# Kernel tuning notes

Hardware: AMD Instinct MI355X
Metric: run time of the kernel (lower is better)

Reference implementation:

```python
import jax, jax.numpy as jnp
import numpy as np

B, V, N = 256, 50, 32
D, H, L, CS, NN, OUT = 128, 384, 12, 10, 10000, 128
ND = N * D          # per-visit input dim
G = 4 * H + 2 * L   # gate projection width
CH = H // L         # chunk size
HS = H // 6         # scale bottleneck


def setup_inputs() -> dict:
    key = jax.random.key(0)
    ks = jax.random.split(key, 20)
    s = 0.02
    embed = jax.random.normal(ks[0], (NN + 1, D), jnp.float32) * s
    embed = embed.at[0].set(0.0)  # padding_idx=0
    inp = {
        'node_ids': jax.random.randint(ks[1], (B, V, N), 0, NN + 1),
        'edge_idx': jax.random.randint(ks[2], (2, 128), 0, NN),
        'edge_attr': jax.random.normal(ks[3], (128,), jnp.float32),
        'time': jax.random.uniform(ks[4], (B, V), jnp.float32),
        'visit_order': jax.random.randint(ks[5], (B, V), 0, V),
        'attn_mask': jnp.ones((B, V), jnp.bool_),
        'embed': embed,
        'kernel_w': jax.random.normal(ks[6], (G, ND + 1), jnp.float32) * s,
        'kernel_b': jnp.zeros((G,), jnp.float32),
        'rec_w': jax.random.normal(ks[7], (G, H + 1), jnp.float32) * s,
        'rec_b': jnp.zeros((G,), jnp.float32),
        'scale_w': jax.random.normal(ks[8], (HS, H), jnp.float32) * s,
        'scale_b': jnp.zeros((HS,), jnp.float32),
        'rescale_w': jax.random.normal(ks[9], (H, HS), jnp.float32) * s,
        'rescale_b': jnp.zeros((H,), jnp.float32),
        'conv_w': jax.random.normal(ks[10], (H, H, CS), jnp.float32) * s,
        'conv_b': jnp.zeros((H,), jnp.float32),
        'out_w': jax.random.normal(ks[11], (OUT, V * H), jnp.float32) * s,
        'out_b': jnp.zeros((OUT,), jnp.float32),
    }
    return inp


def _cumax_l2r(x):
    return jnp.cumsum(jax.nn.softmax(x, -1), -1)


def _cumax_r2l(x):
    return jnp.flip(jnp.cumsum(jax.nn.softmax(jnp.flip(x, -1), -1), -1), -1)


def _forward(node_ids, time, embed, kernel_w, kernel_b, rec_w, rec_b,
             scale_w, scale_b, rescale_w, rescale_b, conv_w, conv_b, out_w, out_b):
    x = embed[node_ids].reshape(B, V, ND)  # gather per-visit code embeddings

    def step(carry, xs):
        c, h, tmp_h, tmp_dis = carry
        x_t, t_t = xs
        iv = t_t[:, None]
        xo = (jnp.concatenate([x_t, iv], -1) @ kernel_w.T + kernel_b
              + jnp.concatenate([h, iv], -1) @ rec_w.T + rec_b)
        fm = _cumax_l2r(xo[:, :L])              # [B,L] master forget
        im = _cumax_r2l(xo[:, L:2 * L])         # [B,L] master input
        g = xo[:, 2 * L:].reshape(B, 4 * L, CH)
        f = jax.nn.sigmoid(g[:, :L])
        i_ = jax.nn.sigmoid(g[:, L:2 * L])
        o = jax.nn.sigmoid(g[:, 2 * L:3 * L])
        cin = jnp.tanh(g[:, 3 * L:])
        cl = c.reshape(B, L, CH)
        fmE, imE = fm[:, :, None], im[:, :, None]
        ov = fmE * imE
        cnew = ov * (f * cl + i_ * cin) + (fmE - ov) * cl + (imE - ov) * cin
        hnew = (o * jnp.tanh(cnew)).reshape(B, H)
        cnew = cnew.reshape(B, H)
        dist = 1.0 - jnp.mean(fm, -1)           # [B]
        tmp_h = jnp.concatenate([tmp_h[1:], hnew[None]], 0)    # [CS,B,H]
        tmp_dis = jnp.concatenate([tmp_dis[1:], dist[None]], 0)  # [CS,B]
        ld = jax.nn.softmax(jnp.cumsum(tmp_dis.T, 1), 1)       # [B,CS]
        lh = tmp_h.transpose(1, 2, 0) * ld[:, None, :]         # [B,H,CS]
        theme = jax.nn.sigmoid(
            jnp.maximum(jnp.mean(lh, -1) @ scale_w.T + scale_b, 0.0)
            @ rescale_w.T + rescale_b)
        conv = jnp.einsum('bhk,ohk->bo', lh, conv_w) + conv_b  # valid conv, len 1
        local = theme * conv
        return (cnew, hnew, tmp_h, tmp_dis), (local, hnew, dist)

    c0 = jnp.zeros((B, H), jnp.float32)
    h0 = jnp.zeros((B, H), jnp.float32)
    tmp_h0 = jnp.zeros((CS, B, H), jnp.float32)
    tmp_dis0 = jnp.zeros((CS, B), jnp.float32)
    xs = (x.transpose(1, 0, 2), time.T)
    _, (hs, ohs, dists) = jax.lax.scan(step, (c0, h0, tmp_h0, tmp_dis0), xs)
    rnn = hs.transpose(1, 0, 2) + ohs.transpose(1, 0, 2)       # [B,V,H]
    out = rnn.reshape(B, V * H) @ out_w.T + out_b
    return out, dists  # dists: [V,B]


def reference(node_ids, edge_idx, edge_attr, time, visit_order, attn_mask,
              embed, kernel_w, kernel_b, rec_w, rec_b, scale_w, scale_b,
              rescale_w, rescale_b, conv_w, conv_b, out_w, out_b):
    # edge_idx / edge_attr / visit_order / attn_mask are unused by StageNet.forward
    return _forward(node_ids, time, embed, kernel_w, kernel_b, rec_w, rec_b,
                    scale_w, scale_b, rescale_w, rescale_b, conv_w, conv_b,
                    out_w, out_b)
```

## Files before the change

### kernel.cpp

```cpp
#include <hip/hip_runtime.h>
#include <math.h>

typedef _Float16 f16;
typedef _Float16 f16x8 __attribute__((ext_vector_type(8)));
typedef float f32x4 __attribute__((ext_vector_type(4)));
typedef unsigned int u32;
typedef u32 u32x4 __attribute__((ext_vector_type(4)));

#define DEV static __device__ __forceinline__

DEV float sigm(float x)  { return 1.0f / (1.0f + __expf(-x)); }
DEV float tanhfast(float x) { return 2.0f / (1.0f + __expf(-2.0f * x)) - 1.0f; }

DEV void gld16(const void* g, void* l) {
  __builtin_amdgcn_global_load_lds((const __attribute__((address_space(1))) void*)g,
                                   (__attribute__((address_space(3))) void*)l, 16, 0, 0);
}

DEV void gbar(int* bar, int nblk) {
  __syncthreads();
  if (threadIdx.x == 0) {
    int* cnt = bar;
    int* gen = bar + 16;
    int g = __hip_atomic_load(gen, __ATOMIC_RELAXED, __HIP_MEMORY_SCOPE_AGENT);
    int a = __hip_atomic_fetch_add(cnt, 1, __ATOMIC_RELEASE, __HIP_MEMORY_SCOPE_AGENT);
    if (a == nblk - 1) {
      __hip_atomic_store(cnt, 0, __ATOMIC_RELAXED, __HIP_MEMORY_SCOPE_AGENT);
      __hip_atomic_store(gen, g + 1, __ATOMIC_RELEASE, __HIP_MEMORY_SCOPE_AGENT);
    } else {
      while (__hip_atomic_load(gen, __ATOMIC_RELAXED, __HIP_MEMORY_SCOPE_AGENT) == g)
        __builtin_amdgcn_s_sleep(1);
    }
    (void)__hip_atomic_load(gen, __ATOMIC_ACQUIRE, __HIP_MEMORY_SCOPE_AGENT);
  }
  __syncthreads();
}

#define GP 1664
#define KH 3840
#define KO 19200
#define ZSPLIT 40
#define NGRP 16
#define NMEM 12
#define NBLK 192
#define XOLS 164
#define RECUR_LDS (122880 + 10496 + 1024)

static constexpr size_t OFF_OPART = 0;
static constexpr size_t OFF_ZB    = 104857600 - 262144;
static constexpr size_t OFF_WK    = 104857600;
static constexpr size_t OFF_XK    = OFF_WK + 13631488;
static constexpr size_t OFF_MLH   = OFF_XK;
static constexpr size_t OFF_S1    = OFF_XK + 9830400;
static constexpr size_t OFF_TH    = OFF_XK + 13107200;
static constexpr size_t OFF_CV    = OFF_XK + 32768000;
static constexpr size_t OFF_SWP   = OFF_XK + 72089600;
static constexpr size_t OFF_RWP2  = OFF_XK + 72187904;
static constexpr size_t OFF_SBP   = OFF_XK + 72286208;
static constexpr size_t OFF_RW    = OFF_XK + 85196800;
static constexpr size_t OFF_SV    = OFF_RW + 1474560;
static constexpr size_t OFF_BAR   = OFF_SV + 8192;
static constexpr size_t OFF_BIASC = OFF_BAR + 32768;
static constexpr size_t OFF_HALL  = OFF_BIASC + 8192;
static constexpr size_t OFF_LD    = OFF_HALL + 9830400;
static constexpr size_t OFF_WC2   = OFF_LD + 512000;
static constexpr size_t OFF_RNN   = OFF_WC2 + 2949120;
static constexpr size_t OFF_OUTW  = OFF_RNN + 9830400;
static constexpr size_t OFF_EH    = OFF_OUTW + 4915200;


__global__ __launch_bounds__(256) void k_prep_wk(const float* __restrict__ kw,
                                                 const float* __restrict__ kb,
                                                 const float* __restrict__ rb,
                                                 f16* __restrict__ Wk,
                                                 float* __restrict__ biasc) {
  long i = (long)blockIdx.x * 256 + threadIdx.x;
  if (i < 1664L * 4096) {
    int nn = (int)(i >> 12);
    int k  = (int)(i & 4095);
    float v = (nn < 1560) ? kw[(long)nn * 4097 + k] : 0.0f;
    Wk[i] = (f16)v;
  }
  if (i < 1664) biasc[i] = (i < 1560) ? (kb[i] + rb[i]) : 0.0f;
}

__global__ __launch_bounds__(512) void k_prep_misc(const float* __restrict__ rw,
                                                   const float* __restrict__ kw,
                                                   const float* __restrict__ sw,
                                                   const float* __restrict__ sb,
                                                   const float* __restrict__ rw2,
                                                   const float* __restrict__ cw,
                                                   const float* __restrict__ ow,
                                                   const float* __restrict__ embed,
                                                   f16* __restrict__ RWp,
                                                   float* __restrict__ Sv,
                                                   int* __restrict__ bar,
                                                   f16* __restrict__ swp,
                                                   float* __restrict__ sbp,
                                                   f16* __restrict__ rwp2,
                                                   f16* __restrict__ Wc2,
                                                   f16* __restrict__ outw,
                                                   f16* __restrict__ Eh) {
  const int blk = blockIdx.x, tid = threadIdx.x;
  if (blk < 180) {
    int i = blk * 512 + tid;
    if (i < 92160) {
      int p = i / 7680;
      int rem = i - p * 7680;
      int tau = rem / 768;
      int r2 = rem - tau * 768;
      int f = r2 >> 6;
      int l = r2 & 63;
      int lc = tau * 16 + (l & 15);
      int n;
      if (lc < 24) n = lc;
      else if (lc < 32) n = -1;
      else { int run = (lc - 32) >> 5; n = 24 + (run * 12 + p) * 32 + ((lc - 32) & 31); }
      int k = f * 32 + ((l >> 4) << 3);
      f16x8 o;
      if (n >= 0) {
        const float* s = rw + (long)n * 385 + k;
#pragma unroll
        for (int e = 0; e < 8; ++e) o[e] = (f16)s[e];
      } else {
#pragma unroll
        for (int e = 0; e < 8; ++e) o[e] = (f16)0.0f;
      }
      *(f16x8*)(RWp + (long)i * 8) = o;
    }
    if (i < 1664)
      Sv[i] = (i < 1560) ? (rw[(long)i * 385 + 384] + kw[(long)i * 4097 + 4096]) : 0.0f;
    if (i < 8192) bar[i] = 0;
  } else if (blk < 276) {
    int i = (blk - 180) * 512 + tid;
    if (i < 128 * 384) {
      int o = i / 384, k = i - o * 384;
      swp[i] = (f16)((o < 64) ? sw[o * 384 + k] : 0.0f);
      int o2 = i >> 7, k2 = i & 127;
      rwp2[i] = (f16)((k2 < 64) ? rw2[o2 * 64 + k2] : 0.0f);
    }
    if (i < 128) sbp[i] = (i < 64) ? sb[i] : 0.0f;
  } else if (blk < 3156) {
    int i = (blk - 276) * 512 + tid;
    if (i < 384 * 3840) {
      int o = i / 3840;
      int c = i - o * 3840;
      int j = c / 384;
      int h = c - j * 384;
      Wc2[i] = (f16)cw[((long)o * 384 + h) * 10 + j];
    }
  } else if (blk < 7956) {
    long i = (long)(blk - 3156) * 512 + tid;
    if (i < 128L * KO) outw[i] = (f16)ow[i];
  } else {
    long i = (long)(blk - 7956) * 512 + tid;
    if (i < 10001L * 128) Eh[i] = (f16)embed[i];
  }
}

__global__ __launch_bounds__(256) void k_gemm_emb(const int* __restrict__ ids,
                                                  const f16* __restrict__ Eh,
                                                  const f16* __restrict__ W,
                                                  f16* __restrict__ C,
                                                  const float* __restrict__ bias) {
  __shared__ __align__(16) f16 As0[128 * 32];
  __shared__ __align__(16) f16 As1[128 * 32];
  __shared__ __align__(16) f16 Bs0[128 * 32];
  __shared__ __align__(16) f16 Bs1[128 * 32];
  const int tid = threadIdx.x;
  const int W0  = blockIdx.y * 100 + blockIdx.x;
  const int xcd = W0 & 7, idx = W0 >> 3;
  const int nw  = (xcd < 4) ? (xcd * 163 + idx) : (652 + (xcd - 4) * 162 + idx);
  const int bx  = nw % 100, by = nw / 100;
  const long rowA0 = (long)bx * 128;
  const long rowB0 = (long)by * 128;
  const int w = tid >> 6, lane = tid & 63;
  const int q = lane >> 4, r16 = lane & 15;
  const int wr = w >> 1, wc = w & 1;
  f32x4 acc[4][4] = {};
  const int srow = tid >> 2;
  const int scol = (tid & 3) * 8;
  const int* idr0 = ids + (rowA0 + srow) * 32;
  const int* idr1 = ids + (rowA0 + srow + 64) * 32;
  const f16* gB0 = W + (rowB0 + srow) * 4096L + scol;
  const f16* gB1 = gB0 + 64L * 4096;
  f16* lA0 = As0 + tid * 8;
  f16* lA1 = As1 + tid * 8;
  f16* lB0 = Bs0 + tid * 8;
  f16* lB1 = Bs1 + tid * 8;
  int cur0 = idr0[0], cur1 = idr1[0];
  for (int n = 0; n < 32; ++n) {
    int nx0 = 0, nx1 = 0;
    if (n < 31) { nx0 = idr0[n + 1]; nx1 = idr1[n + 1]; }
#pragma unroll
    for (int kk = 0; kk < 2; ++kk) {
      const int k0 = n * 128 + kk * 64;
      const int d = kk * 64 + scol;
      __syncthreads();
      gld16(Eh + (size_t)cur0 * 128 + d,      lA0);
      gld16(Eh + (size_t)cur1 * 128 + d,      lA0 + 2048);
      gld16(Eh + (size_t)cur0 * 128 + d + 32, lA1);
      gld16(Eh + (size_t)cur1 * 128 + d + 32, lA1 + 2048);
      gld16(gB0 + k0,      lB0);
      gld16(gB1 + k0,      lB0 + 2048);
      gld16(gB0 + k0 + 32, lB1);
      gld16(gB1 + k0 + 32, lB1 + 2048);
      __syncthreads();
      f16x8 af[4], bfr[4];
#pragma unroll
      for (int i = 0; i < 4; i++) {
        af[i]  = *(const f16x8*)&As0[(wr * 64 + i * 16 + r16) * 32 + q * 8];
        bfr[i] = *(const f16x8*)&Bs0[(wc * 64 + i * 16 + r16) * 32 + q * 8];
      }
#pragma unroll
      for (int i = 0; i < 4; i++)
#pragma unroll
        for (int j = 0; j < 4; j++)
          acc[i][j] = __builtin_amdgcn_mfma_f32_16x16x32_f16(af[i], bfr[j], acc[i][j], 0, 0, 0);
#pragma unroll
      for (int i = 0; i < 4; i++) {
        af[i]  = *(const f16x8*)&As1[(wr * 64 + i * 16 + r16) * 32 + q * 8];
        bfr[i] = *(const f16x8*)&Bs1[(wc * 64 + i * 16 + r16) * 32 + q * 8];
      }
#pragma unroll
      for (int i = 0; i < 4; i++)
#pragma unroll
        for (int j = 0; j < 4; j++)
          acc[i][j] = __builtin_amdgcn_mfma_f32_16x16x32_f16(af[i], bfr[j], acc[i][j], 0, 0, 0);
    }
    cur0 = nx0; cur1 = nx1;
  }
#pragma unroll
  for (int i = 0; i < 4; i++)
#pragma unroll
    for (int j = 0; j < 4; j++) {
      long row = rowA0 + wr * 64 + i * 16 + q * 4;
      long col = rowB0 + wc * 64 + j * 16 + r16;
      float bv = bias[col];
#pragma unroll
      for (int r = 0; r < 4; r++)
        C[(row + r) * (long)GP + col] = (f16)(acc[i][j][r] + bv);
    }
}

__global__ __launch_bounds__(256) void k_gemm_conv(const float* __restrict__ ld,
                                                   const f16* __restrict__ h_all,
                                                   const f16* __restrict__ W,
                                                   float* __restrict__ C) {
  __shared__ __align__(16) f16 As[128 * 32];
  __shared__ __align__(16) f16 Bs[128 * 32];
  const int tid = threadIdx.x;
  const long rowA0 = (long)blockIdx.x * 128;
  const long rowB0 = (long)blockIdx.y * 128;
  const int ks = blockIdx.z * 1920;
  const long zoff = (long)blockIdx.z * (12800L * 384);
  const int w = tid >> 6, lane = tid & 63;
  const int q = lane >> 4, r16 = lane & 15;
  const int wr = w >> 1, wc = w & 1;
  f32x4 acc[4][4] = {};
  const int srow = tid >> 2;
  const int scol = (tid & 3) * 8;
  const int row0 = (int)rowA0 + srow, row1 = row0 + 64;
  const int b0r = row0 / 50, t0r = row0 - b0r * 50;
  const int b1r = row1 / 50, t1r = row1 - b1r * 50;
  const f16* gB0 = W + (rowB0 + srow) * (long)KH + ks + scol;
  const f16* gB1 = gB0 + 64L * KH;
  f16* lB = Bs + tid * 8;
  for (int k0 = 0; k0 < 1920; k0 += 32) {
    const int col0 = ks + k0;
    const int j = col0 / 384;
    const int hh = col0 - j * 384 + scol;
    const int s0 = t0r - 9 + j, s1 = t1r - 9 + j;
    __syncthreads();
    gld16(gB0 + k0, lB);
    gld16(gB1 + k0, lB + 2048);
    f16x8 a0v = {}, a1v = {};
    if (s0 >= 0) {
      const float lv = ld[row0 * 10 + j];
      f16x8 hv = *(const f16x8*)(h_all + ((size_t)s0 * 256 + b0r) * 384 + hh);
#pragma unroll
      for (int e = 0; e < 8; ++e) a0v[e] = (f16)((float)hv[e] * lv);
    }
    if (s1 >= 0) {
      const float lv = ld[row1 * 10 + j];
      f16x8 hv = *(const f16x8*)(h_all + ((size_t)s1 * 256 + b1r) * 384 + hh);
#pragma unroll
      for (int e = 0; e < 8; ++e) a1v[e] = (f16)((float)hv[e] * lv);
    }
    *(f16x8*)&As[srow * 32 + scol] = a0v;
    *(f16x8*)&As[(srow + 64) * 32 + scol] = a1v;
    __syncthreads();
    f16x8 af[4], bfr[4];
#pragma unroll
    for (int i = 0; i < 4; i++) {
      af[i]  = *(const f16x8*)&As[(wr * 64 + i * 16 + r16) * 32 + q * 8];
      bfr[i] = *(const f16x8*)&Bs[(wc * 64 + i * 16 + r16) * 32 + q * 8];
    }
#pragma unroll
    for (int i = 0; i < 4; i++)
#pragma unroll
      for (int j2 = 0; j2 < 4; j2++)
        acc[i][j2] = __builtin_amdgcn_mfma_f32_16x16x32_f16(af[i], bfr[j2], acc[i][j2], 0, 0, 0);
  }
#pragma unroll
  for (int i = 0; i < 4; i++)
#pragma unroll
    for (int j2 = 0; j2 < 4; j2++) {
      long row = rowA0 + wr * 64 + i * 16 + q * 4;
      long col = rowB0 + wc * 64 + j2 * 16 + r16;
#pragma unroll
      for (int r = 0; r < 4; r++)
        C[(row + r) * 384L + col + zoff] = acc[i][j2][r];
    }
}

__global__ __launch_bounds__(256) void k_gemm_bt(const f16* __restrict__ A,
                                                 const f16* __restrict__ W,
                                                 void* __restrict__ Cv,
                                                 const float* __restrict__ bias,
                                                 int N, int K, int kLen, int act) {
  __shared__ __align__(16) f16 As[128 * 32];
  __shared__ __align__(16) f16 Bs[128 * 32];
  const int tid = threadIdx.x;
  const long rowA0 = (long)blockIdx.x * 128;
  const long rowB0 = (long)blockIdx.y * 128;
  const long ks = (long)blockIdx.z * kLen;
  const long zoff = (long)blockIdx.z * ((long)gridDim.x * 128 * N);
  const int w = tid >> 6, lane = tid & 63;
  const int q = lane >> 4, r16 = lane & 15;
  const int wr = w >> 1, wc = w & 1;
  f32x4 acc[4][4] = {};
  const int srow = tid >> 2;
  const int scol = (tid & 3) * 8;
  const f16* gA0 = A + (rowA0 + srow) * (long)K + ks + scol;
  const f16* gA1 = gA0 + 64L * K;
  const f16* gB0 = W + (rowB0 + srow) * (long)K + ks + scol;
  const f16* gB1 = gB0 + 64L * K;
  f16* lA = As + tid * 8;
  f16* lB = Bs + tid * 8;
  for (int k0 = 0; k0 < kLen; k0 += 32) {
    __syncthreads();
    gld16(gA0 + k0, lA);
    gld16(gA1 + k0, lA + 2048);
    gld16(gB0 + k0, lB);
    gld16(gB1 + k0, lB + 2048);
    __syncthreads();
    f16x8 af[4], bfr[4];
#pragma unroll
    for (int i = 0; i < 4; i++) {
      af[i]  = *(const f16x8*)&As[(wr * 64 + i * 16 + r16) * 32 + q * 8];
      bfr[i] = *(const f16x8*)&Bs[(wc * 64 + i * 16 + r16) * 32 + q * 8];
    }
#pragma unroll
    for (int i = 0; i < 4; i++)
#pragma unroll
      for (int j = 0; j < 4; j++)
        acc[i][j] = __builtin_amdgcn_mfma_f32_16x16x32_f16(af[i], bfr[j], acc[i][j], 0, 0, 0);
  }
#pragma unroll
  for (int i = 0; i < 4; i++)
#pragma unroll
    for (int j = 0; j < 4; j++) {
      long row = rowA0 + wr * 64 + i * 16 + q * 4;
      long col = rowB0 + wc * 64 + j * 16 + r16;
      float bv = bias ? bias[col] : 0.0f;
#pragma unroll
      for (int r = 0; r < 4; r++) {
        float v = acc[i][j][r] + bv;
        long off = (row + r) * (long)N + col + zoff;
        if (act == 0)      ((float*)Cv)[off] = v;
        else if (act == 1) ((f16*)Cv)[off]   = (f16)v;
        else if (act == 2) ((f16*)Cv)[off]   = (f16)fmaxf(v, 0.0f);
        else               ((float*)Cv)[off] = sigm(v);
      }
    }
}

__global__ __launch_bounds__(640)
void k_recur_coop(const f16* __restrict__ XKh,
                  const f16* __restrict__ RWp,
                  const float* __restrict__ Sv,
                  const float* __restrict__ timep,
                  f16* __restrict__ zbuf,
                  f16* __restrict__ hall,
                  float* __restrict__ dists,
                  int* __restrict__ bar) {
  extern __shared__ char smem[];
  f16*   Wl  = (f16*)smem;
  float* xol = (float*)(smem + 122880);
  f16*   hl  = (f16*)(smem + 122880 + 10496);
  const int tid = threadIdx.x;
  const int g = blockIdx.x / NMEM;
  const int m = blockIdx.x - g * NMEM;
  const int b0 = g * 16;
  int* gflags = bar + g * 256;
  int* ibar   = bar + 4096 + g * 32;
  const int w = tid >> 6, lane = tid & 63;
  const int q = lane >> 4, r16 = lane & 15;
  {
    const f16* src = RWp + (size_t)m * 61440;
    for (int i = tid; i < 7680; i += 640)
      *(f16x8*)(Wl + (size_t)i * 8) = *(const f16x8*)(src + (size_t)i * 8);
  }
  int ncol = -1; float Svc = 0.0f;
  if (w < 10) {
    const int lc = w * 16 + r16;
    if (lc < 24) ncol = lc;
    else if (lc >= 32) { int run = (lc - 32) >> 5; ncol = 24 + (run * 12 + m) * 32 + ((lc - 32) & 31); }
    if (ncol >= 0) Svc = Sv[ncol];
  }
  {
    f16x8 z = {};
    for (int i = m * 640 + tid; i < 768; i += NMEM * 640)
      *(f16x8*)(zbuf + (size_t)b0 * 384 + (size_t)i * 8) = z;
  }
  gbar(ibar, NMEM);

  const int ch = tid & 31, bloc = tid >> 5;
  float creg = 0.0f;
  f16 xkc[4] = {};
  if (w < 10 && ncol >= 0) {
#pragma unroll
    for (int r = 0; r < 4; ++r)
      xkc[r] = XKh[((long)(b0 + q * 4 + r) * 50) * GP + ncol];
  }

  for (int t = 0; t < 50; ++t) {
    const f16* hprev = (t == 0) ? zbuf : (hall + (size_t)(t - 1) * 98304);
    f16 xkn[4] = {};
    if (w < 10) {
      f16x8 af[12];
      const f16* ab = hprev + (size_t)(b0 + r16) * 384 + q * 8;
#pragma unroll
      for (int f = 0; f < 12; ++f) af[f] = *(const f16x8*)(ab + f * 32);
      if (t < 49 && ncol >= 0) {
#pragma unroll
        for (int r = 0; r < 4; ++r)
          xkn[r] = XKh[((long)(b0 + q * 4 + r) * 50 + (t + 1)) * GP + ncol];
      }
      float tv4[4];
#pragma unroll
      for (int r = 0; r < 4; ++r) tv4[r] = timep[(b0 + q * 4 + r) * 50 + t];
      const f16* bp = Wl + (size_t)w * 6144 + lane * 8;
      f32x4 a0 = {};
#pragma unroll
      for (int f = 0; f < 12; ++f)
        a0 = __builtin_amdgcn_mfma_f32_16x16x32_f16(af[f], *(const f16x8*)(bp + f * 512), a0, 0, 0, 0);
      const int lc = w * 16 + r16;
#pragma unroll
      for (int r = 0; r < 4; ++r)
        xol[(q * 4 + r) * XOLS + lc] = a0[r] + (float)xkc[r] + tv4[r] * Svc;
    }
    __syncthreads();
    if (bloc < 16) {
      const int gb = b0 + bloc;
      const float* xr = xol + bloc * XOLS;
      float e1[12], e2[12], mx1 = -1e30f, mx2 = -1e30f;
#pragma unroll
      for (int l = 0; l < 12; ++l) {
        e1[l] = xr[l];      mx1 = fmaxf(mx1, e1[l]);
        e2[l] = xr[12 + l]; mx2 = fmaxf(mx2, e2[l]);
      }
      float s1 = 0.0f, s2 = 0.0f;
#pragma unroll
      for (int l = 0; l < 12; ++l) {
        e1[l] = __expf(e1[l] - mx1); s1 += e1[l];
        e2[l] = __expf(e2[l] - mx2); s2 += e2[l];
      }
      float cum1 = 0.0f;
      for (int l = 0; l <= m; ++l) cum1 += e1[l];
      const float fmv = cum1 / s1;
      float cum2 = 0.0f;
      for (int l = 11; l >= m; --l) cum2 += e2[l];
      const float imv = cum2 / s2;
      if (m == 0 && ch == 0) {
        float ds = 0.0f;
#pragma unroll
        for (int l = 0; l < 12; ++l) ds += (float)(12 - l) * e1[l];
        dists[t * 256 + gb] = 1.0f - ds / (12.0f * s1);
      }
      const float fv = sigm(xr[32 + ch]);
      const float iv = sigm(xr[64 + ch]);
      const float og = sigm(xr[96 + ch]);
      const float ci = tanhfast(xr[128 + ch]);
      const float ov = fmv * imv;
      const float cn = ov * (fv * creg + iv * ci) + (fmv - ov) * creg + (imv - ov) * ci;
      creg = cn;
      const float hv = og * tanhfast(cn);
      hl[tid] = (f16)hv;
    }
    __syncthreads();
    if (w == 0) {
      f32x4 d = *(const f32x4*)(hl + lane * 8);
      f16* dst = hall + ((size_t)t * 256 + b0 + (lane >> 2)) * 384 + m * 32 + (lane & 3) * 8;
      asm volatile("global_store_dwordx4 %0, %1, off sc0 sc1\n\t"
                   "s_waitcnt vmcnt(0)"
                   :: "v"(dst), "v"(d) : "memory");
      if (lane == 0) {
        int* fp = gflags + m * 16;
        int fv2 = t + 1;
        asm volatile("global_store_dword %0, %1, off sc0 sc1"
                     :: "v"(fp), "v"(fv2) : "memory");
      }
    }
    if (w == 1 && lane < NMEM) {
      while (__hip_atomic_load(gflags + lane * 16, __ATOMIC_RELAXED, __HIP_MEMORY_SCOPE_AGENT) < t + 1)
        __builtin_amdgcn_s_sleep(1);
    }
    __syncthreads();
    asm volatile("" ::: "memory");
#pragma unroll
    for (int r = 0; r < 4; ++r) xkc[r] = xkn[r];
  }
}

__global__ __launch_bounds__(256) void k_ld(const float* __restrict__ dists,
                                            float* __restrict__ ld) {
  int i = blockIdx.x * 256 + threadIdx.x;
  if (i >= 12800) return;
  int b = i / 50, t = i - b * 50;
  float v[10];
  float cum = 0.0f, mx = -1e30f;
#pragma unroll
  for (int j = 0; j < 10; j++) {
    int s = t - 9 + j;
    float d = (s >= 0) ? dists[s * 256 + b] : 0.0f;
    cum += d; v[j] = cum; mx = fmaxf(mx, cum);
  }
  float sum = 0.0f;
#pragma unroll
  for (int j = 0; j < 10; j++) { v[j] = __expf(v[j] - mx); sum += v[j]; }
  float inv = 1.0f / sum;
#pragma unroll
  for (int j = 0; j < 10; j++) ld[i * 10 + j] = v[j] * inv;
}

__global__ __launch_bounds__(256) void k_mlh(const float* __restrict__ ld,
                                             const f16* __restrict__ h_all,
                                             f16* __restrict__ mlh) {
  int i = blockIdx.x * 256 + threadIdx.x;
  int row = i / 384, h = i - row * 384;
  int b = row / 50, t = row - b * 50;
  float acc = 0.0f;
#pragma unroll
  for (int j = 0; j < 10; j++) {
    int s = t - 9 + j;
    if (s >= 0) acc += ld[row * 10 + j] * (float)h_all[((size_t)s * 256 + b) * 384 + h];
  }
  mlh[i] = (f16)(acc * 0.1f);
}

__global__ __launch_bounds__(256) void k_rnn(const float* __restrict__ theme,
                                             const float* __restrict__ convp,
                                             const float* __restrict__ cb,
                                             const f16* __restrict__ h_all,
                                             f16* __restrict__ rnn) {
  int i = blockIdx.x * 256 + threadIdx.x;
  int row = i / 384, h = i - row * 384;
  int b = row / 50, t = row - b * 50;
  float conv = convp[i] + convp[4915200 + i] + cb[h];
  float local = theme[i] * conv;
  float hv = (float)h_all[((size_t)t * 256 + b) * 384 + h];
  rnn[i] = (f16)(local + hv);
}

__global__ __launch_bounds__(256) void k_red(const float* __restrict__ part,
                                             const float* __restrict__ ob,
                                             float* __restrict__ out) {
  int i = blockIdx.x * 256 + threadIdx.x;
  float s = 0.0f;
#pragma unroll
  for (int z = 0; z < ZSPLIT; z++) s += part[z * 32768 + i];
  out[i] = s + ob[i & 127];
}

extern "C" void kernel_launch(void* const* d_in, const int* in_sizes, int n_in,
                              void* d_out, int out_size, void* d_ws, size_t ws_size,
                              hipStream_t stream) {
  (void)in_sizes; (void)n_in; (void)out_size; (void)ws_size;
  const int*   node_ids  = (const int*)  d_in[0];
  const float* timep     = (const float*)d_in[3];
  const float* embed     = (const float*)d_in[6];
  const float* kernel_w  = (const float*)d_in[7];
  const float* kernel_b  = (const float*)d_in[8];
  const float* rec_w     = (const float*)d_in[9];
  const float* rec_b     = (const float*)d_in[10];
  const float* scale_w   = (const float*)d_in[11];
  const float* scale_b   = (const float*)d_in[12];
  const float* rescale_w = (const float*)d_in[13];
  const float* rescale_b = (const float*)d_in[14];
  const float* conv_w    = (const float*)d_in[15];
  const float* conv_b    = (const float*)d_in[16];
  const float* out_w     = (const float*)d_in[17];
  const float* out_b     = (const float*)d_in[18];

  char* ws = (char*)d_ws;
  float* opart   = (float*)(ws + OFF_OPART);
  f16*   zbuf    = (f16*)  (ws + OFF_ZB);
  f16*   Wk      = (f16*)  (ws + OFF_WK);
  f16*   XKh     = (f16*)  (ws + OFF_XK);
  f16*   mlh_h   = (f16*)  (ws + OFF_MLH);
  f16*   s1h     = (f16*)  (ws + OFF_S1);
  float* theme   = (float*)(ws + OFF_TH);
  float* convbuf = (float*)(ws + OFF_CV);
  f16*   swp     = (f16*)  (ws + OFF_SWP);
  f16*   rwp2    = (f16*)  (ws + OFF_RWP2);
  float* sbp     = (float*)(ws + OFF_SBP);
  f16*   RWp     = (f16*)  (ws + OFF_RW);
  float* Sv      = (float*)(ws + OFF_SV);
  int*   bar     = (int*)  (ws + OFF_BAR);
  float* biasc   = (float*)(ws + OFF_BIASC);
  f16*   h_all   = (f16*)  (ws + OFF_HALL);
  float* ldbuf   = (float*)(ws + OFF_LD);
  f16*   Wc2     = (f16*)  (ws + OFF_WC2);
  f16*   rnn     = (f16*)  (ws + OFF_RNN);
  f16*   outw    = (f16*)  (ws + OFF_OUTW);
  f16*   Eh      = (f16*)  (ws + OFF_EH);

  float* outp  = (float*)d_out;
  float* dists = outp + 256 * 128;

  k_prep_wk  <<<26624, 256, 0, stream>>>(kernel_w, kernel_b, rec_b, Wk, biasc);
  k_prep_misc<<<10457, 512, 0, stream>>>(rec_w, kernel_w, scale_w, scale_b, rescale_w,
                                         conv_w, out_w, embed,
                                         RWp, Sv, bar, swp, sbp, rwp2, Wc2, outw, Eh);
  k_gemm_emb<<<dim3(100, 13), 256, 0, stream>>>(node_ids, Eh, Wk, XKh, biasc);
  {
    hipFuncSetAttribute((const void*)k_recur_coop,
                        hipFuncAttributeMaxDynamicSharedMemorySize, RECUR_LDS);
    void* cargs[] = {(void*)&XKh, (void*)&RWp, (void*)&Sv, (void*)&timep,
                     (void*)&zbuf, (void*)&h_all, (void*)&dists, (void*)&bar};
    hipLaunchCooperativeKernel((void*)k_recur_coop, dim3(NBLK), dim3(640),
                               cargs, RECUR_LDS, stream);
  }
  k_ld  <<<50,    256, 0, stream>>>(dists, ldbuf);
  k_mlh <<<19200, 256, 0, stream>>>(ldbuf, h_all, mlh_h);
  k_gemm_bt<<<dim3(100, 1), 256, 0, stream>>>(mlh_h, swp, s1h, sbp, 128, 384, 384, 2);
  k_gemm_bt<<<dim3(100, 3), 256, 0, stream>>>(s1h, rwp2, theme, rescale_b, 384, 128, 128, 3);
  k_gemm_conv<<<dim3(100, 3, 2), 256, 0, stream>>>(ldbuf, h_all, Wc2, convbuf);
  k_rnn <<<19200, 256, 0, stream>>>(theme, convbuf, conv_b, h_all, rnn);
  k_gemm_bt<<<dim3(2, 1, ZSPLIT), 256, 0, stream>>>(rnn, outw, opart, nullptr, 128, KO, KO / ZSPLIT, 0);
  k_red<<<128, 256, 0, stream>>>(opart, out_b, outp);
}
```

Measured before the change: 936.8 us.

## Replace cooperative multi-block recurrence with single-block-per-batch-group fused kernel

The recurrent scan previously split each 16-row batch group across 12 cooperating blocks, which exchanged h through global memory with flag-based inter-block synchronisation every timestep. It now gives each group one 1024-thread block that holds the entire recurrent weight matrix in registers (78 f16x8 per thread) and keeps h in LDS. The weight prep is re-laid out so each wave owns a column slice and a K half, and the two K halves are reduced through LDS. This removes the global-memory h round trip and the cross-block spin-waits, but launches only 16 blocks and puts heavy register pressure on each thread.

```diff
diff --git a/kernel.cpp b/kernel.cpp
--- a/kernel.cpp
+++ b/kernel.cpp
@@ -17,37 +17,15 @@
                                    (__attribute__((address_space(3))) void*)l, 16, 0, 0);
 }
 
-DEV void gbar(int* bar, int nblk) {
-  __syncthreads();
-  if (threadIdx.x == 0) {
-    int* cnt = bar;
-    int* gen = bar + 16;
-    int g = __hip_atomic_load(gen, __ATOMIC_RELAXED, __HIP_MEMORY_SCOPE_AGENT);
-    int a = __hip_atomic_fetch_add(cnt, 1, __ATOMIC_RELEASE, __HIP_MEMORY_SCOPE_AGENT);
-    if (a == nblk - 1) {
-      __hip_atomic_store(cnt, 0, __ATOMIC_RELAXED, __HIP_MEMORY_SCOPE_AGENT);
-      __hip_atomic_store(gen, g + 1, __ATOMIC_RELEASE, __HIP_MEMORY_SCOPE_AGENT);
-    } else {
-      while (__hip_atomic_load(gen, __ATOMIC_RELAXED, __HIP_MEMORY_SCOPE_AGENT) == g)
-        __builtin_amdgcn_s_sleep(1);
-    }
-    (void)__hip_atomic_load(gen, __ATOMIC_ACQUIRE, __HIP_MEMORY_SCOPE_AGENT);
-  }
-  __syncthreads();
-}
-
 #define GP 1664
 #define KH 3840
 #define KO 19200
 #define ZSPLIT 40
-#define NGRP 16
-#define NMEM 12
-#define NBLK 192
-#define XOLS 164
-#define RECUR_LDS (122880 + 10496 + 1024)
+#define XOLN 1668
+#define HPAD 392
+#define FUSED_LDS (106752 + 12544 + 6656 + 1536)
 
 static constexpr size_t OFF_OPART = 0;
-static constexpr size_t OFF_ZB    = 104857600 - 262144;
 static constexpr size_t OFF_WK    = 104857600;
 static constexpr size_t OFF_XK    = OFF_WK + 13631488;
 static constexpr size_t OFF_MLH   = OFF_XK;
@@ -92,7 +70,7 @@
                                                    const float* __restrict__ cw,
                                                    const float* __restrict__ ow,
                                                    const float* __restrict__ embed,
-                                                   f16* __restrict__ RWp,
+                                                   f16* __restrict__ RWn,
                                                    float* __restrict__ Sv,
                                                    int* __restrict__ bar,
                                                    f16* __restrict__ swp,
@@ -104,29 +82,23 @@
   const int blk = blockIdx.x, tid = threadIdx.x;
   if (blk < 180) {
     int i = blk * 512 + tid;
-    if (i < 92160) {
-      int p = i / 7680;
-      int rem = i - p * 7680;
-      int tau = rem / 768;
-      int r2 = rem - tau * 768;
-      int f = r2 >> 6;
-      int l = r2 & 63;
-      int lc = tau * 16 + (l & 15);
-      int n;
-      if (lc < 24) n = lc;
-      else if (lc < 32) n = -1;
-      else { int run = (lc - 32) >> 5; n = 24 + (run * 12 + p) * 32 + ((lc - 32) & 31); }
-      int k = f * 32 + ((l >> 4) << 3);
+    if (i < 79872) {
+      int w2   = i / 4992;
+      int rem  = i - w2 * 4992;
+      int f    = rem >> 6;
+      int lane = rem & 63;
+      int col  = (w2 >> 1) * 208 + (f / 6) * 16 + (lane & 15);
+      int kk   = ((w2 & 1) * 6 + (f % 6)) * 32 + ((lane >> 4) << 3);
       f16x8 o;
-      if (n >= 0) {
-        const float* s = rw + (long)n * 385 + k;
+      if (col < 1560) {
+        const float* s = rw + (long)col * 385 + kk;
 #pragma unroll
         for (int e = 0; e < 8; ++e) o[e] = (f16)s[e];
       } else {
 #pragma unroll
         for (int e = 0; e < 8; ++e) o[e] = (f16)0.0f;
       }
-      *(f16x8*)(RWp + (long)i * 8) = o;
+      *(f16x8*)(RWn + (long)i * 8) = o;
     }
     if (i < 1664)
       Sv[i] = (i < 1560) ? (rw[(long)i * 385 + 384] + kw[(long)i * 4097 + 4096]) : 0.0f;
@@ -376,141 +348,132 @@
     }
 }
 
-__global__ __launch_bounds__(640)
-void k_recur_coop(const f16* __restrict__ XKh,
-                  const f16* __restrict__ RWp,
-                  const float* __restrict__ Sv,
-                  const float* __restrict__ timep,
-                  f16* __restrict__ zbuf,
-                  f16* __restrict__ hall,
-                  float* __restrict__ dists,
-                  int* __restrict__ bar) {
+__global__ __launch_bounds__(1024, 1)
+void k_recur_fused(const f16* __restrict__ XKh,
+                   const f16* __restrict__ RWn,
+                   const float* __restrict__ Sv,
+                   const float* __restrict__ timep,
+                   f16* __restrict__ hall,
+                   float* __restrict__ dists) {
   extern __shared__ char smem[];
-  f16*   Wl  = (f16*)smem;
-  float* xol = (float*)(smem + 122880);
-  f16*   hl  = (f16*)(smem + 122880 + 10496);
+  float* xol  = (float*)smem;
+  f16*   hbuf = (f16*)(smem + 106752);
+  float* svl  = (float*)(smem + 106752 + 12544);
+  float* fml  = (float*)(smem + 106752 + 12544 + 6656);
+  float* iml  = fml + 192;
   const int tid = threadIdx.x;
-  const int g = blockIdx.x / NMEM;
-  const int m = blockIdx.x - g * NMEM;
-  const int b0 = g * 16;
-  int* gflags = bar + g * 256;
-  int* ibar   = bar + 4096 + g * 32;
+  const int b0 = blockIdx.x * 16;
   const int w = tid >> 6, lane = tid & 63;
   const int q = lane >> 4, r16 = lane & 15;
+  const int cs = w >> 1, kh = w & 1;
+
+  f16x8 wv[78];
   {
-    const f16* src = RWp + (size_t)m * 61440;
-    for (int i = tid; i < 7680; i += 640)
-      *(f16x8*)(Wl + (size_t)i * 8) = *(const f16x8*)(src + (size_t)i * 8);
-  }
-  int ncol = -1; float Svc = 0.0f;
-  if (w < 10) {
-    const int lc = w * 16 + r16;
-    if (lc < 24) ncol = lc;
-    else if (lc >= 32) { int run = (lc - 32) >> 5; ncol = 24 + (run * 12 + m) * 32 + ((lc - 32) & 31); }
-    if (ncol >= 0) Svc = Sv[ncol];
-  }
-  {
-    f16x8 z = {};
-    for (int i = m * 640 + tid; i < 768; i += NMEM * 640)
-      *(f16x8*)(zbuf + (size_t)b0 * 384 + (size_t)i * 8) = z;
-  }
-  gbar(ibar, NMEM);
-
-  const int ch = tid & 31, bloc = tid >> 5;
-  float creg = 0.0f;
-  f16 xkc[4] = {};
-  if (w < 10 && ncol >= 0) {
-#pragma unroll
-    for (int r = 0; r < 4; ++r)
-      xkc[r] = XKh[((long)(b0 + q * 4 + r) * 50) * GP + ncol];
-  }
+    const f16* src = RWn + ((size_t)w * 4992 + lane) * 8;
+#pragma unroll
+    for (int f = 0; f < 78; ++f)
+      wv[f] = *(const f16x8*)(src + (size_t)f * 512);
+  }
+  for (int i = tid; i < 1664; i += 1024) svl[i] = Sv[i];
+  for (int i = tid; i < 16 * HPAD; i += 1024) hbuf[i] = (f16)0.0f;
+
+  const int gb = tid >> 6;
+  const int gc = tid & 63;
+  float creg[6] = {};
+  __syncthreads();
 
   for (int t = 0; t < 50; ++t) {
-    const f16* hprev = (t == 0) ? zbuf : (hall + (size_t)(t - 1) * 98304);
-    f16 xkn[4] = {};
-    if (w < 10) {
-      f16x8 af[12];
-      const f16* ab = hprev + (size_t)(b0 + r16) * 384 + q * 8;
-#pragma unroll
-      for (int f = 0; f < 12; ++f) af[f] = *(const f16x8*)(ab + f * 32);
-      if (t < 49 && ncol >= 0) {
-#pragma unroll
-        for (int r = 0; r < 4; ++r)
-          xkn[r] = XKh[((long)(b0 + q * 4 + r) * 50 + (t + 1)) * GP + ncol];
-      }
-      float tv4[4];
-#pragma unroll
-      for (int r = 0; r < 4; ++r) tv4[r] = timep[(b0 + q * 4 + r) * 50 + t];
-      const f16* bp = Wl + (size_t)w * 6144 + lane * 8;
-      f32x4 a0 = {};
-#pragma unroll
-      for (int f = 0; f < 12; ++f)
-        a0 = __builtin_amdgcn_mfma_f32_16x16x32_f16(af[f], *(const f16x8*)(bp + f * 512), a0, 0, 0, 0);
-      const int lc = w * 16 + r16;
-#pragma unroll
-      for (int r = 0; r < 4; ++r)
-        xol[(q * 4 + r) * XOLS + lc] = a0[r] + (float)xkc[r] + tv4[r] * Svc;
-    }
-    __syncthreads();
-    if (bloc < 16) {
-      const int gb = b0 + bloc;
-      const float* xr = xol + bloc * XOLS;
+    const f16* xrow = XKh + ((size_t)(b0 + gb) * 50 + t) * GP;
+    f16 xkg[4][6];
+#pragma unroll
+    for (int G = 0; G < 4; ++G)
+#pragma unroll
+      for (int j = 0; j < 6; ++j)
+        xkg[G][j] = xrow[24 + G * 384 + gc + j * 64];
+    const float tvb = timep[(b0 + gb) * 50 + t];
+
+    f16x8 af[6];
+#pragma unroll
+    for (int i = 0; i < 6; ++i)
+      af[i] = *(const f16x8*)(hbuf + r16 * HPAD + (kh * 6 + i) * 32 + q * 8);
+    f32x4 acc[13];
+#pragma unroll
+    for (int j = 0; j < 13; ++j) acc[j] = (f32x4){0.f, 0.f, 0.f, 0.f};
+#pragma unroll
+    for (int j = 0; j < 13; ++j)
+#pragma unroll
+      for (int i = 0; i < 6; ++i)
+        acc[j] = __builtin_amdgcn_mfma_f32_16x16x32_f16(af[i], wv[j * 6 + i], acc[j], 0, 0, 0);
+    if (kh == 0) {
+#pragma unroll
+      for (int j = 0; j < 13; ++j) {
+        const int col = cs * 208 + j * 16 + r16;
+#pragma unroll
+        for (int rr = 0; rr < 4; ++rr)
+          xol[(q * 4 + rr) * XOLN + col] = acc[j][rr];
+      }
+    }
+    __syncthreads();
+    if (kh == 1) {
+#pragma unroll
+      for (int j = 0; j < 13; ++j) {
+        const int col = cs * 208 + j * 16 + r16;
+#pragma unroll
+        for (int rr = 0; rr < 4; ++rr)
+          xol[(q * 4 + rr) * XOLN + col] += acc[j][rr];
+      }
+    }
+    __syncthreads();
+    if (tid < 192) {
+      const int b = tid / 12, l = tid - (tid / 12) * 12;
+      const f16* xr2 = XKh + ((size_t)(b0 + b) * 50 + t) * GP;
+      const float tv2 = timep[(b0 + b) * 50 + t];
       float e1[12], e2[12], mx1 = -1e30f, mx2 = -1e30f;
 #pragma unroll
-      for (int l = 0; l < 12; ++l) {
-        e1[l] = xr[l];      mx1 = fmaxf(mx1, e1[l]);
-        e2[l] = xr[12 + l]; mx2 = fmaxf(mx2, e2[l]);
-      }
-      float s1 = 0.0f, s2 = 0.0f;
-#pragma unroll
-      for (int l = 0; l < 12; ++l) {
-        e1[l] = __expf(e1[l] - mx1); s1 += e1[l];
-        e2[l] = __expf(e2[l] - mx2); s2 += e2[l];
-      }
-      float cum1 = 0.0f;
-      for (int l = 0; l <= m; ++l) cum1 += e1[l];
-      const float fmv = cum1 / s1;
-      float cum2 = 0.0f;
-      for (int l = 11; l >= m; --l) cum2 += e2[l];
-      const float imv = cum2 / s2;
-      if (m == 0 && ch == 0) {
-        float ds = 0.0f;
-#pragma unroll
-        for (int l = 0; l < 12; ++l) ds += (float)(12 - l) * e1[l];
-        dists[t * 256 + gb] = 1.0f - ds / (12.0f * s1);
-      }
-      const float fv = sigm(xr[32 + ch]);
-      const float iv = sigm(xr[64 + ch]);
-      const float og = sigm(xr[96 + ch]);
-      const float ci = tanhfast(xr[128 + ch]);
+      for (int c = 0; c < 12; ++c) {
+        e1[c] = xol[b * XOLN + c] + (float)xr2[c] + tv2 * svl[c];
+        mx1 = fmaxf(mx1, e1[c]);
+        e2[c] = xol[b * XOLN + 12 + c] + (float)xr2[12 + c] + tv2 * svl[12 + c];
+        mx2 = fmaxf(mx2, e2[c]);
+      }
+      float s1 = 0.f, s2 = 0.f;
+#pragma unroll
+      for (int c = 0; c < 12; ++c) {
+        e1[c] = __expf(e1[c] - mx1); s1 += e1[c];
+        e2[c] = __expf(e2[c] - mx2); s2 += e2[c];
+      }
+      float cum1 = 0.f;
+      for (int c = 0; c <= l; ++c) cum1 += e1[c];
+      fml[b * 12 + l] = cum1 / s1;
+      float cum2 = 0.f;
+      for (int c = 11; c >= l; --c) cum2 += e2[c];
+      iml[b * 12 + l] = cum2 / s2;
+      if (l == 0) {
+        float ds = 0.f;
+#pragma unroll
+        for (int c = 0; c < 12; ++c) ds += (float)(12 - c) * e1[c];
+        dists[t * 256 + b0 + b] = 1.0f - ds / (12.0f * s1);
+      }
+    }
+    __syncthreads();
+#pragma unroll
+    for (int j = 0; j < 6; ++j) {
+      const int ch = gc + j * 64;
+      const int l = ch >> 5;
+      const float fv = sigm(xol[gb * XOLN + 24 + ch]        + (float)xkg[0][j] + tvb * svl[24 + ch]);
+      const float iv = sigm(xol[gb * XOLN + 24 + 384 + ch]  + (float)xkg[1][j] + tvb * svl[24 + 384 + ch]);
+      const float og = sigm(xol[gb * XOLN + 24 + 768 + ch]  + (float)xkg[2][j] + tvb * svl[24 + 768 + ch]);
+      const float ci = tanhfast(xol[gb * XOLN + 24 + 1152 + ch] + (float)xkg[3][j] + tvb * svl[24 + 1152 + ch]);
+      const float fmv = fml[gb * 12 + l];
+      const float imv = iml[gb * 12 + l];
       const float ov = fmv * imv;
-      const float cn = ov * (fv * creg + iv * ci) + (fmv - ov) * creg + (imv - ov) * ci;
-      creg = cn;
+      const float cn = ov * (fv * creg[j] + iv * ci) + (fmv - ov) * creg[j] + (imv - ov) * ci;
+      creg[j] = cn;
       const float hv = og * tanhfast(cn);
-      hl[tid] = (f16)hv;
-    }
-    __syncthreads();
-    if (w == 0) {
-      f32x4 d = *(const f32x4*)(hl + lane * 8);
-      f16* dst = hall + ((size_t)t * 256 + b0 + (lane >> 2)) * 384 + m * 32 + (lane & 3) * 8;
-      asm volatile("global_store_dwordx4 %0, %1, off sc0 sc1\n\t"
-                   "s_waitcnt vmcnt(0)"
-                   :: "v"(dst), "v"(d) : "memory");
-      if (lane == 0) {
-        int* fp = gflags + m * 16;
-        int fv2 = t + 1;
-        asm volatile("global_store_dword %0, %1, off sc0 sc1"
-                     :: "v"(fp), "v"(fv2) : "memory");
-      }
-    }
-    if (w == 1 && lane < NMEM) {
-      while (__hip_atomic_load(gflags + lane * 16, __ATOMIC_RELAXED, __HIP_MEMORY_SCOPE_AGENT) < t + 1)
-        __builtin_amdgcn_s_sleep(1);
-    }
-    __syncthreads();
-    asm volatile("" ::: "memory");
-#pragma unroll
-    for (int r = 0; r < 4; ++r) xkc[r] = xkn[r];
+      hbuf[gb * HPAD + ch] = (f16)hv;
+      hall[((size_t)t * 256 + b0 + gb) * 384 + ch] = (f16)hv;
+    }
+    __syncthreads();
   }
 }
 
@@ -596,7 +559,6 @@
 
   char* ws = (char*)d_ws;
   float* opart   = (float*)(ws + OFF_OPART);
-  f16*   zbuf    = (f16*)  (ws + OFF_ZB);
   f16*   Wk      = (f16*)  (ws + OFF_WK);
   f16*   XKh     = (f16*)  (ws + OFF_XK);
   f16*   mlh_h   = (f16*)  (ws + OFF_MLH);
@@ -606,7 +568,7 @@
   f16*   swp     = (f16*)  (ws + OFF_SWP);
   f16*   rwp2    = (f16*)  (ws + OFF_RWP2);
   float* sbp     = (float*)(ws + OFF_SBP);
-  f16*   RWp     = (f16*)  (ws + OFF_RW);
+  f16*   RWn     = (f16*)  (ws + OFF_RW);
   float* Sv      = (float*)(ws + OFF_SV);
   int*   bar     = (int*)  (ws + OFF_BAR);
   float* biasc   = (float*)(ws + OFF_BIASC);
@@ -623,15 +585,12 @@
   k_prep_wk  <<<26624, 256, 0, stream>>>(kernel_w, kernel_b, rec_b, Wk, biasc);
   k_prep_misc<<<10457, 512, 0, stream>>>(rec_w, kernel_w, scale_w, scale_b, rescale_w,
                                          conv_w, out_w, embed,
-                                         RWp, Sv, bar, swp, sbp, rwp2, Wc2, outw, Eh);
+                                         RWn, Sv, bar, swp, sbp, rwp2, Wc2, outw, Eh);
   k_gemm_emb<<<dim3(100, 13), 256, 0, stream>>>(node_ids, Eh, Wk, XKh, biasc);
   {
-    hipFuncSetAttribute((const void*)k_recur_coop,
-                        hipFuncAttributeMaxDynamicSharedMemorySize, RECUR_LDS);
-    void* cargs[] = {(void*)&XKh, (void*)&RWp, (void*)&Sv, (void*)&timep,
-                     (void*)&zbuf, (void*)&h_all, (void*)&dists, (void*)&bar};
-    hipLaunchCooperativeKernel((void*)k_recur_coop, dim3(NBLK), dim3(640),
-                               cargs, RECUR_LDS, stream);
+    hipFuncSetAttribute((const void*)k_recur_fused,
+                        hipFuncAttributeMaxDynamicSharedMemorySize, FUSED_LDS);
+    k_recur_fused<<<16, 1024, FUSED_LDS, stream>>>(XKh, RWn, Sv, timep, h_all, dists);
   }
   k_ld  <<<50,    256, 0, stream>>>(dists, ldbuf);
   k_mlh <<<19200, 256, 0, stream>>>(ldbuf, h_all, mlh_h);
```

New measurement: 2.706 ms. 189% more time.
